# Kernel tuning notes

Measured on AMD Instinct MI355X. Metric: run time of the kernel, lower is better.

## Reference

```python
import jax, jax.numpy as jnp
import numpy as np

HIDDEN = 2048
NUM_HEADS = 16
NUM_KV_HEADS = 4
HEAD_DIM = HIDDEN // NUM_HEADS  # 128
WINDOW = 512
THETA = 10000.0
BATCH = 4
SEQ = 2048
NEG = -1e30


def _apply_rope(x, pos, theta):
    # x: [T, H, D] with interleaved even/odd rotation, matching the torch strided slicing
    half = x.shape[-1] // 2
    inv_freq = 1.0 / (theta ** (jnp.arange(half, dtype=jnp.float32) / half))
    ang = pos.astype(jnp.float32)[:, None] * inv_freq[None, :]          # [T, half]
    cos = jnp.cos(ang)[:, None, :]                                       # [T, 1, half]
    sin = jnp.sin(ang)[:, None, :]
    xe = x[..., 0::2].astype(jnp.float32)
    xo = x[..., 1::2].astype(jnp.float32)
    re = xe * cos - xo * sin
    ro = xe * sin + xo * cos
    out = jnp.stack([re, ro], axis=-1).reshape(x.shape)                  # re-interleave
    return out.astype(x.dtype)


def setup_inputs() -> dict:
    key = jax.random.key(0)
    ks = jax.random.split(key, 5)
    sc = 1.0 / np.sqrt(HIDDEN)
    hidden_states = jax.random.normal(ks[0], (BATCH * SEQ, HIDDEN), dtype=jnp.float32)
    q_w = jax.random.normal(ks[1], (HIDDEN, NUM_HEADS * HEAD_DIM), dtype=jnp.float32) * sc
    k_w = jax.random.normal(ks[2], (HIDDEN, NUM_KV_HEADS * HEAD_DIM), dtype=jnp.float32) * sc
    v_w = jax.random.normal(ks[3], (HIDDEN, NUM_KV_HEADS * HEAD_DIM), dtype=jnp.float32) * sc
    o_w = jax.random.normal(ks[4], (HIDDEN, HIDDEN), dtype=jnp.float32) * sc
    position_ids = jnp.tile(jnp.arange(SEQ, dtype=jnp.int32), BATCH)     # restart per sequence
    cu_seqlens = jnp.arange(BATCH + 1, dtype=jnp.int32) * SEQ
    return {
        "hidden_states": hidden_states, "q_w": q_w, "k_w": k_w, "v_w": v_w, "o_w": o_w,
        "position_ids": position_ids, "cu_seqlens": cu_seqlens, "max_seq_len": SEQ,
    }


def reference(hidden_states, q_w, k_w, v_w, o_w, position_ids, cu_seqlens, max_seq_len):
    T = hidden_states.shape[0]
    B = cu_seqlens.shape[0] - 1
    S = T // B  # equal-length packing
    groups = NUM_HEADS // NUM_KV_HEADS

    q = (hidden_states @ q_w).reshape(T, NUM_HEADS, HEAD_DIM)
    k = (hidden_states @ k_w).reshape(T, NUM_KV_HEADS, HEAD_DIM)
    v = (hidden_states @ v_w).reshape(T, NUM_KV_HEADS, HEAD_DIM)

    q = _apply_rope(q, position_ids, THETA)
    k = _apply_rope(k, position_ids, THETA)

    q = q.reshape(B, S, NUM_HEADS, HEAD_DIM)
    k = k.reshape(B, S, NUM_KV_HEADS, HEAD_DIM)
    v = v.reshape(B, S, NUM_KV_HEADS, HEAD_DIM)
    # GQA: expand kv heads to query heads
    k = jnp.repeat(k, groups, axis=2)   # [B, S, H, D]
    v = jnp.repeat(v, groups, axis=2)

    scale = 1.0 / np.sqrt(HEAD_DIM)
    scores = jnp.einsum('bqhd,bkhd->bhqk', q, k) * scale  # [B, H, S, S]

    pos = position_ids.reshape(B, S)
    pq = pos[:, None, :, None]
    pk = pos[:, None, None, :]
    # causal + sliding window (flash window_size=(WINDOW, 0) semantics): q-k in [0, WINDOW]
    allowed = (pk <= pq) & ((pq - pk) <= WINDOW)
    scores = jnp.where(allowed, scores, NEG)

    probs = jax.nn.softmax(scores, axis=-1)
    attn = jnp.einsum('bhqk,bkhd->bqhd', probs, v)        # [B, S, H, D]
    attn = attn.reshape(T, HIDDEN)
    return attn @ o_w
```

## Files before the change

### kernel.cpp

```cpp
#include <hip/hip_runtime.h>
#include <hip/hip_bf16.h>
#include <cstdint>
#include <cstddef>

typedef __bf16 bf16;
typedef __bf16 bf16x2 __attribute__((ext_vector_type(2)));
typedef __bf16 bf16x8 __attribute__((ext_vector_type(8)));
typedef float  f32x4  __attribute__((ext_vector_type(4)));

#define HIDDEN 2048
#define NHEADS 16
#define NKV    4
#define HD     128
#define WINDOW 512
#define NLT    -0.14390747054172642f

__device__ __forceinline__ void gld16(const void* g, void* s) {
  __builtin_amdgcn_global_load_lds((const __attribute__((address_space(1))) void*)g,
                                   (__attribute__((address_space(3))) void*)s, 16, 0, 0);
}

__device__ __forceinline__ f32x4 mfma16(bf16x8 a, bf16x8 b, f32x4 c) {
  return __builtin_amdgcn_mfma_f32_16x16x32_bf16(a, b, c, 0, 0, 0);
}

__device__ __forceinline__ void barrier_raw() {
  asm volatile("" ::: "memory");
  __builtin_amdgcn_s_barrier();
  asm volatile("" ::: "memory");
}

__global__ __launch_bounds__(256) void cast_f32_bf16(const float* __restrict__ in,
                                                     bf16* __restrict__ out, int n4) {
  int i = blockIdx.x * 256 + threadIdx.x;
  if (i >= n4) return;
  f32x4 v = *(const f32x4*)(in + (size_t)i * 4);
  bf16x2 a, b;
  a[0] = (bf16)v[0]; a[1] = (bf16)v[1];
  b[0] = (bf16)v[2]; b[1] = (bf16)v[3];
  *(bf16x2*)(out + (size_t)i * 4)     = a;
  *(bf16x2*)(out + (size_t)i * 4 + 2) = b;
}

__global__ __launch_bounds__(256) void transpose_cast2(const float* __restrict__ in0,
                                                       bf16* __restrict__ out0,
                                                       const float* __restrict__ in1,
                                                       bf16* __restrict__ out1,
                                                       int R, int C) {
  const float* in = blockIdx.z ? in1 : in0;
  bf16* out       = blockIdx.z ? out1 : out0;
  __shared__ float tile[32][33];
  int c0 = blockIdx.x * 32, r0 = blockIdx.y * 32;
  int tx = threadIdx.x, ty = threadIdx.y;
  #pragma unroll
  for (int i = 0; i < 4; ++i)
    tile[ty + i * 8][tx] = in[(size_t)(r0 + ty + i * 8) * C + c0 + tx];
  __syncthreads();
  #pragma unroll
  for (int i = 0; i < 4; ++i)
    out[(size_t)(c0 + ty + i * 8) * R + r0 + tx] = (bf16)tile[tx][ty + i * 8];
}

__device__ __forceinline__ void stage128x64(const bf16* __restrict__ A,
                                            const bf16* __restrict__ Bt,
                                            bf16* sA, bf16* sB,
                                            int m0, int n0, int K, int kt, int tid) {
  int wb = (tid & ~63) * 8;
  #pragma unroll
  for (int r = 0; r < 4; ++r) {
    int n = r * 256 + tid;
    int row = n >> 3;
    int c = (n & 7) ^ (row & 7);
    gld16(A  + (size_t)(m0 + row) * K + (size_t)kt * 64 + c * 8,
          sA + (size_t)(r * 256 * 8) + wb);
    gld16(Bt + (size_t)(n0 + row) * K + (size_t)kt * 64 + c * 8,
          sB + (size_t)(r * 256 * 8) + wb);
  }
}

__global__ __launch_bounds__(256) void gemm_bt(const bf16* __restrict__ A,
                                               const bf16* __restrict__ Bt,
                                               void* __restrict__ Cv,
                                               bf16* __restrict__ Vtout,
                                               const int* __restrict__ pos,
                                               int M, int N, int K, int outMode) {
  __shared__ bf16 sA[2][128 * 64];
  __shared__ bf16 sB[2][128 * 64];
  int nb = N >> 7;
  int perx = (int)gridDim.x >> 3;
  int bid0 = (int)blockIdx.x;
  int swzb = (bid0 & 7) * perx + (bid0 >> 3);
  int bm = swzb / nb, bn = swzb % nb;
  int m0 = bm << 7, n0 = bn << 7;
  int tid = threadIdx.x;
  int lane = tid & 63, w = tid >> 6;
  int li = lane & 15, g = lane >> 4;
  int wm = w >> 1, wn = w & 1;
  int swz = li & 7;
  f32x4 acc[4][4] = {};
  int NT = K >> 6;

  stage128x64(A, Bt, sA[0], sB[0], m0, n0, K, 0, tid);
  for (int kt = 0; kt < NT; ++kt) {
    int cur = kt & 1;
    asm volatile("s_waitcnt vmcnt(0)" ::: "memory");
    barrier_raw();
    if (kt + 1 < NT)
      stage128x64(A, Bt, sA[cur ^ 1], sB[cur ^ 1], m0, n0, K, kt + 1, tid);
    bf16x8 af[4][2], bv[4][2];
    #pragma unroll
    for (int mt = 0; mt < 4; ++mt)
      #pragma unroll
      for (int ks = 0; ks < 2; ++ks)
        af[mt][ks] = *(const bf16x8*)&sA[cur][(wm * 64 + mt * 16 + li) * 64
                                              + ((ks * 4 + g) ^ swz) * 8];
    #pragma unroll
    for (int nt = 0; nt < 4; ++nt)
      #pragma unroll
      for (int ks = 0; ks < 2; ++ks)
        bv[nt][ks] = *(const bf16x8*)&sB[cur][(wn * 64 + nt * 16 + li) * 64
                                              + ((ks * 4 + g) ^ swz) * 8];
    #pragma unroll
    for (int mt = 0; mt < 4; ++mt)
      #pragma unroll
      for (int nt = 0; nt < 4; ++nt)
        #pragma unroll
        for (int ks = 0; ks < 2; ++ks)
          acc[mt][nt] = mfma16(af[mt][ks], bv[nt][ks], acc[mt][nt]);
  }
  #pragma unroll
  for (int mt = 0; mt < 4; ++mt)
    #pragma unroll
    for (int nt = 0; nt < 4; ++nt)
      #pragma unroll
      for (int j = 0; j < 4; ++j) {
        int row = m0 + wm * 64 + mt * 16 + g * 4 + j;
        int col = n0 + wn * 64 + nt * 16 + li;
        float v = acc[mt][nt][j];
        if (outMode == 0)      ((bf16*)Cv)[(size_t)row * N + col] = (bf16)v;
        else if (outMode == 1) ((bf16*)Cv)[(size_t)col * M + row] = (bf16)v;
        else if (outMode == 2) ((float*)Cv)[(size_t)row * N + col] = v;
        else {
          if (col < 512) {
            float inv = __expf((float)((col & 127) >> 1) * NLT);
            float ang = (float)pos[row] * inv;
            float s = __sinf(ang), c = __cosf(ang);
            float pv = __shfl_xor(v, 1);
            float outv = (li & 1) ? (pv * s + v * c) : (v * c - pv * s);
            ((bf16*)Cv)[(size_t)row * 512 + col] = (bf16)outv;
          } else {
            Vtout[(size_t)(col - 512) * M + row] = (bf16)v;
          }
        }
      }
}

template<int RSP>
__device__ __forceinline__ void stage_quad(const bf16* __restrict__ G,
                                           bf16* __restrict__ sbuf,
                                           int grow0, int K, int k0, int half, int tid) {
  int w = tid >> 6, lane = tid & 63;
  int rl = lane >> 3;
  int col = ((lane & 7) ^ rl) * 8;
  #pragma unroll
  for (int r = 0; r < 2; ++r) {
    int lr0 = r * 64 + w * 8;
    int row0 = (lr0 & (RSP - 1)) + half * RSP + (lr0 / RSP) * 2 * RSP;
    gld16(G + (size_t)(grow0 + row0 + rl) * K + k0 + col,
          sbuf + row0 * 64);
  }
}

__global__ __launch_bounds__(512, 2) void gemm256(const bf16* __restrict__ A,
                                                  const bf16* __restrict__ Bt,
                                                  void* __restrict__ Cv,
                                                  const int* __restrict__ pos,
                                                  int M, int N, int K, int outMode) {
  __shared__ bf16 sA[2][256 * 64];
  __shared__ bf16 sB[2][256 * 64];
  int nb = N >> 8;
  int cpx = (int)gridDim.x >> 3;
  int bid = (int)blockIdx.x;
  int swzb = (bid & 7) * cpx + (bid >> 3);
  int bm = swzb / nb, bn = swzb % nb;
  int m0 = bm << 8, n0 = bn << 8;
  int tid = threadIdx.x, lane = tid & 63, w = tid >> 6;
  int li = lane & 15, g = lane >> 4;
  int wm = w >> 2, wn = w & 3;
  int swz = (li & 7);

  f32x4 acc[8][4] = {};
  bf16x8 af[4][2];
  bf16x8 bv[2][2][2];

  int NT = K >> 6;

  stage_quad<64>(A,  sA[0], m0, K, 0, 0, tid);
  stage_quad<32>(Bt, sB[0], n0, K, 0, 0, tid);
  stage_quad<32>(Bt, sB[0], n0, K, 0, 1, tid);
  stage_quad<64>(A,  sA[0], m0, K, 0, 1, tid);

#define VMW(n) asm volatile("s_waitcnt vmcnt(" #n ")" ::: "memory")
#define SBAR() __builtin_amdgcn_sched_barrier(0)
#define LGKM(n) { asm volatile("s_waitcnt lgkmcnt(" #n ")" ::: "memory"); \
  __builtin_amdgcn_sched_barrier(0); }
#define LOAD_A256(mh) { _Pragma("unroll") for (int mf = 0; mf < 4; ++mf) \
  _Pragma("unroll") for (int ks = 0; ks < 2; ++ks) { \
    int row = wm * 128 + (mh) * 64 + mf * 16 + li; \
    af[mf][ks] = *(const bf16x8*)&sA[cur][row * 64 + ((ks * 4 + g) ^ swz) * 8]; } }
#define LOAD_B256(nh) { _Pragma("unroll") for (int nf = 0; nf < 2; ++nf) \
  _Pragma("unroll") for (int ks = 0; ks < 2; ++ks) { \
    int row = wn * 64 + (nh) * 32 + nf * 16 + li; \
    bv[nh][nf][ks] = *(const bf16x8*)&sB[cur][row * 64 + ((ks * 4 + g) ^ swz) * 8]; } }
#define MFMA_PH(mh, nh) { \
  __builtin_amdgcn_s_setprio(1); \
  _Pragma("unroll") for (int mf = 0; mf < 4; ++mf) \
  _Pragma("unroll") for (int nf = 0; nf < 2; ++nf) \
  _Pragma("unroll") for (int ks = 0; ks < 2; ++ks) \
    acc[(mh) * 4 + mf][(nh) * 2 + nf] = \
      mfma16(af[mf][ks], bv[nh][nf][ks], acc[(mh) * 4 + mf][(nh) * 2 + nf]); \
  __builtin_amdgcn_s_setprio(0); }

  int cur = 0;
  for (int t = 0; t < NT; ++t) {
    int nxt = cur ^ 1;
    bool pre = (t + 1 < NT);
    int k1 = (t + 1) << 6;
    VMW(0);
    barrier_raw();
    if (pre) stage_quad<64>(A, sA[nxt], m0, K, k1, 0, tid);
    LOAD_A256(0); LOAD_B256(0);
    SBAR();
    LOAD_B256(1);
    if (pre) stage_quad<32>(Bt, sB[nxt], n0, K, k1, 0, tid);
    LGKM(4);
    MFMA_PH(0, 0);
    if (pre) stage_quad<32>(Bt, sB[nxt], n0, K, k1, 1, tid);
    LGKM(0);
    MFMA_PH(0, 1);
    LOAD_A256(1);
    if (pre) stage_quad<64>(A, sA[nxt], m0, K, k1, 1, tid);
    LGKM(0);
    MFMA_PH(1, 1);
    MFMA_PH(1, 0);
    cur = nxt;
  }
#undef VMW
#undef SBAR
#undef LGKM
#undef LOAD_A256
#undef LOAD_B256
#undef MFMA_PH

  if (outMode == 3) {
    float inv4[4];
    #pragma unroll
    for (int ni = 0; ni < 4; ++ni) {
      int col = n0 + wn * 64 + ni * 16 + li;
      inv4[ni] = __expf((float)((col & 127) >> 1) * NLT);
    }
    #pragma unroll
    for (int mi = 0; mi < 8; ++mi)
      #pragma unroll
      for (int j = 0; j < 4; ++j) {
        int row = m0 + wm * 128 + mi * 16 + g * 4 + j;
        float pr = (float)pos[row];
        #pragma unroll
        for (int ni = 0; ni < 4; ++ni) {
          int col = n0 + wn * 64 + ni * 16 + li;
          float ang = pr * inv4[ni];
          float s = __sinf(ang), c = __cosf(ang);
          float v = acc[mi][ni][j];
          float pv = __shfl_xor(v, 1);
          float outv = (li & 1) ? (pv * s + v * c) : (v * c - pv * s);
          ((bf16*)Cv)[(size_t)row * N + col] = (bf16)outv;
        }
      }
  } else {
    #pragma unroll
    for (int mi = 0; mi < 8; ++mi)
      #pragma unroll
      for (int ni = 0; ni < 4; ++ni)
        #pragma unroll
        for (int j = 0; j < 4; ++j) {
          int row = m0 + wm * 128 + mi * 16 + g * 4 + j;
          int col = n0 + wn * 64 + ni * 16 + li;
          float v = acc[mi][ni][j];
          if (outMode == 2) ((float*)Cv)[(size_t)row * N + col] = v;
          else              ((bf16*)Cv)[(size_t)row * N + col] = (bf16)v;
        }
  }
}

__global__ __launch_bounds__(512) void attn_kernel(const bf16* __restrict__ Q,
                                                   const bf16* __restrict__ Kb,
                                                   const bf16* __restrict__ Vt,
                                                   const int* __restrict__ pos,
                                                   const int* __restrict__ cu,
                                                   bf16* __restrict__ O, int T, int B) {
  __shared__ bf16 sK[2][64 * 128];
  __shared__ bf16 sV[2][128 * 64];
  __shared__ bf16 sP[8][16 * 40];
  int bid = blockIdx.x;
  int nqb = T >> 6;
  int kvh = bid / nqb;
  int u   = bid % nqb;
  int qb  = (u & 7) * (nqb >> 3) + (u >> 3);
  int q0 = qb * 64;
  int tid = threadIdx.x, lane = tid & 63, w = tid >> 6;
  int hh = w & 3, rh = w >> 2;
  int h = kvh * 4 + hh;
  int li = lane & 15, g = lane >> 4, g8 = g * 8;
  int rb0 = q0 + rh * 32;

  int seq_start = 0, seq_end = T;
  for (int b = 0; b < B; ++b) {
    int a = cu[b], e = cu[b + 1];
    if (q0 >= a && q0 < e) { seq_start = a; seq_end = e; }
  }

  bf16x8 qf[2][4];
  #pragma unroll
  for (int grp = 0; grp < 2; ++grp)
    #pragma unroll
    for (int kd = 0; kd < 4; ++kd)
      qf[grp][kd] = *(const bf16x8*)(Q + (size_t)(rb0 + grp * 16 + li) * HIDDEN
                                     + h * HD + kd * 32 + g8);

  int pq[2][4], pmin[2], pmax[2];
  #pragma unroll
  for (int grp = 0; grp < 2; ++grp) {
    #pragma unroll
    for (int j = 0; j < 4; ++j) pq[grp][j] = pos[rb0 + grp * 16 + g * 4 + j];
    pmin[grp] = pos[rb0 + grp * 16];
    pmax[grp] = pos[rb0 + grp * 16 + 15];
  }

  float lsum[2][4] = {};
  f32x4 acc[2][8] = {};
  int kstart = q0 - WINDOW;
  if (kstart < seq_start) kstart = seq_start;
  int kend = q0 + 64;
  if (kend > seq_end) kend = seq_end;
  const float scale = 0.08838834764831845f;
  int nt = (kend - kstart) >> 6;

#define STAGE(kb_, buf_) { \
  _Pragma("unroll") for (int r = 0; r < 2; ++r) { \
    int n = r * 512 + tid; \
    int krow = n >> 4, kc = (n & 15) ^ (krow & 7); \
    gld16(Kb + (size_t)((kb_) + krow) * (NKV * HD) + kvh * HD + kc * 8, \
          &sK[buf_][(size_t)(r * 512 + (tid & ~63)) * 8]); \
    int vd = n >> 3, vc = (n & 7) ^ (vd & 7); \
    gld16(Vt + (size_t)(kvh * HD + vd) * T + (kb_) + vc * 8, \
          &sV[buf_][(size_t)(r * 512 + (tid & ~63)) * 8]); } }
#define VMW(n) asm volatile("s_waitcnt vmcnt(" #n ")" ::: "memory")

  STAGE(kstart, 0);
  for (int t = 0; t < nt; ++t) {
    int kb0 = kstart + t * 64;
    int cur = t & 1;
    VMW(0);
    barrier_raw();
    if (t + 1 < nt) STAGE(kb0 + 64, cur ^ 1);

    #pragma unroll
    for (int hhalf = 0; hhalf < 2; ++hhalf) {
      int kb = kb0 + hhalf * 32;
      int pkf = pos[kb], pkl = pos[kb + 31];
      int pk0 = pos[kb + li], pk1 = pos[kb + 16 + li];
      #pragma unroll
      for (int grp = 0; grp < 2; ++grp) {
        if (pkf > pmax[grp] || pkl < pmin[grp] - WINDOW) continue;
        f32x4 s0v = {0.f, 0.f, 0.f, 0.f}, s1v = {0.f, 0.f, 0.f, 0.f};
        #pragma unroll
        for (int kd = 0; kd < 4; ++kd) {
          int c0 = (kd * 4 + g) ^ (li & 7);
          bf16x8 b0 = *(const bf16x8*)&sK[cur][(hhalf * 32 + li) * 128 + c0 * 8];
          bf16x8 b1 = *(const bf16x8*)&sK[cur][(hhalf * 32 + 16 + li) * 128 + c0 * 8];
          s0v = mfma16(qf[grp][kd], b0, s0v);
          s1v = mfma16(qf[grp][kd], b1, s1v);
        }
        bool interior = (pkl <= pmin[grp]) && (pmax[grp] - pkf <= WINDOW);
        if (interior) {
          #pragma unroll
          for (int j = 0; j < 4; ++j) {
            float p0 = __expf(s0v[j] * scale);
            float p1 = __expf(s1v[j] * scale);
            lsum[grp][j] += p0 + p1;
            sP[w][(g * 4 + j) * 40 + li]      = (bf16)p0;
            sP[w][(g * 4 + j) * 40 + 16 + li] = (bf16)p1;
          }
        } else {
          #pragma unroll
          for (int j = 0; j < 4; ++j) {
            int d0 = pq[grp][j] - pk0, d1 = pq[grp][j] - pk1;
            float p0 = (d0 >= 0 && d0 <= WINDOW) ? __expf(s0v[j] * scale) : 0.f;
            float p1 = (d1 >= 0 && d1 <= WINDOW) ? __expf(s1v[j] * scale) : 0.f;
            lsum[grp][j] += p0 + p1;
            sP[w][(g * 4 + j) * 40 + li]      = (bf16)p0;
            sP[w][(g * 4 + j) * 40 + 16 + li] = (bf16)p1;
          }
        }
        bf16x8 pa = *(const bf16x8*)&sP[w][li * 40 + g8];
        #pragma unroll
        for (int dt = 0; dt < 8; ++dt) {
          int d = dt * 16 + li;
          int vc2 = (hhalf * 4 + g) ^ (d & 7);
          bf16x8 vf = *(const bf16x8*)&sV[cur][d * 64 + vc2 * 8];
          acc[grp][dt] = mfma16(pa, vf, acc[grp][dt]);
        }
      }
    }
  }
#undef STAGE
#undef VMW

  #pragma unroll
  for (int grp = 0; grp < 2; ++grp)
    #pragma unroll
    for (int j = 0; j < 4; ++j) {
      float rs = lsum[grp][j];
      rs += __shfl_xor(rs, 1);
      rs += __shfl_xor(rs, 2);
      rs += __shfl_xor(rs, 4);
      rs += __shfl_xor(rs, 8);
      float invl = 1.0f / rs;
      size_t base = (size_t)(rb0 + grp * 16 + g * 4 + j) * HIDDEN + h * HD;
      #pragma unroll
      for (int dt = 0; dt < 8; ++dt)
        O[base + dt * 16 + li] = (bf16)(acc[grp][dt][j] * invl);
    }
}

extern "C" void kernel_launch(void* const* d_in, const int* in_sizes, int n_in,
                              void* d_out, int out_size, void* d_ws, size_t ws_size,
                              hipStream_t stream) {
  const float* X  = (const float*)d_in[0];
  const float* qw = (const float*)d_in[1];
  const float* kw = (const float*)d_in[2];
  const float* vw = (const float*)d_in[3];
  const float* ow = (const float*)d_in[4];
  const int* pos = (const int*)d_in[5];
  const int* cu  = (const int*)d_in[6];
  int T = in_sizes[0] / HIDDEN;
  int B = in_sizes[6] - 1;
  float* out = (float*)d_out;

  bf16* ws = (bf16*)d_ws;
  size_t off = 0;
  bf16* Xb    = ws + off; off += (size_t)T * HIDDEN;
  bf16* Qb    = ws + off; off += (size_t)T * HIDDEN;
  bf16* Kb    = ws + off; off += (size_t)T * (NKV * HD);
  bf16* Vt    = ws + off; off += (size_t)T * (NKV * HD);
  bf16* qwT   = ws + off; off += (size_t)HIDDEN * HIDDEN;
  bf16* kvwT  = ws + off; off += (size_t)1024 * HIDDEN;
  bf16* owT   = ws + off; off += (size_t)HIDDEN * HIDDEN;

  cast_f32_bf16<<<(T * HIDDEN / 4 + 255) / 256, 256, 0, stream>>>(X, Xb, T * HIDDEN / 4);

  dim3 tb(32, 8);
  transpose_cast2<<<dim3(HIDDEN / 32, HIDDEN / 32, 2), tb, 0, stream>>>(
      qw, qwT, ow, owT, HIDDEN, HIDDEN);
  transpose_cast2<<<dim3(512 / 32, HIDDEN / 32, 2), tb, 0, stream>>>(
      kw, kvwT, vw, kvwT + (size_t)512 * HIDDEN, HIDDEN, 512);

  gemm256<<<(T / 256) * (HIDDEN / 256), 512, 0, stream>>>(Xb, qwT, Qb, pos,
                                                          T, HIDDEN, HIDDEN, 3);
  gemm_bt<<<(T / 128) * (1024 / 128), 256, 0, stream>>>(Xb, kvwT, Kb, Vt, pos,
                                                        T, 1024, HIDDEN, 3);

  attn_kernel<<<(T / 64) * NKV, 512, 0, stream>>>(Qb, Kb, Vt, pos, cu, Qb, T, B);

  gemm256<<<(T / 256) * (HIDDEN / 256), 512, 0, stream>>>(Qb, owT, out, nullptr,
                                                          T, HIDDEN, HIDDEN, 2);
}
```

Measured before the change: 282.6 us.

## Vectorize cast and epilogue stores, issue all gemm256 prefetches up front

Several changes land together. The f32-to-bf16 cast now handles 8 elements per thread with one 16-byte store, and the gemm_bt epilogue splits by column range. The V part writes 4 contiguous bf16 with one vector store, and the RoPE parts pair neighbouring lanes into bf16x2 stores. The gemm256 main loop now issues all four next-tile global-to-LDS stage loads at the start of each iteration, instead of interleaving them between MFMA phases. This aims to cut the number of narrow stores and to start prefetching earlier, at the risk of bunching memory traffic ahead of the MFMA work.

After: 292.3 us. 3.4% more time.

```diff
diff --git a/kernel.cpp b/kernel.cpp
--- a/kernel.cpp
+++ b/kernel.cpp
@@ -5,6 +5,7 @@
 
 typedef __bf16 bf16;
 typedef __bf16 bf16x2 __attribute__((ext_vector_type(2)));
+typedef __bf16 bf16x4 __attribute__((ext_vector_type(4)));
 typedef __bf16 bf16x8 __attribute__((ext_vector_type(8)));
 typedef float  f32x4  __attribute__((ext_vector_type(4)));
 
@@ -31,15 +32,15 @@
 }
 
 __global__ __launch_bounds__(256) void cast_f32_bf16(const float* __restrict__ in,
-                                                     bf16* __restrict__ out, int n4) {
+                                                     bf16* __restrict__ out, int n8) {
   int i = blockIdx.x * 256 + threadIdx.x;
-  if (i >= n4) return;
-  f32x4 v = *(const f32x4*)(in + (size_t)i * 4);
-  bf16x2 a, b;
-  a[0] = (bf16)v[0]; a[1] = (bf16)v[1];
-  b[0] = (bf16)v[2]; b[1] = (bf16)v[3];
-  *(bf16x2*)(out + (size_t)i * 4)     = a;
-  *(bf16x2*)(out + (size_t)i * 4 + 2) = b;
+  if (i >= n8) return;
+  f32x4 a = *(const f32x4*)(in + (size_t)i * 8);
+  f32x4 b = *(const f32x4*)(in + (size_t)i * 8 + 4);
+  bf16x8 o;
+  #pragma unroll
+  for (int k = 0; k < 4; ++k) { o[k] = (bf16)a[k]; o[k + 4] = (bf16)b[k]; }
+  *(bf16x8*)(out + (size_t)i * 8) = o;
 }
 
 __global__ __launch_bounds__(256) void transpose_cast2(const float* __restrict__ in0,
@@ -128,31 +129,54 @@
         for (int ks = 0; ks < 2; ++ks)
           acc[mt][nt] = mfma16(af[mt][ks], bv[nt][ks], acc[mt][nt]);
   }
-  #pragma unroll
-  for (int mt = 0; mt < 4; ++mt)
-    #pragma unroll
-    for (int nt = 0; nt < 4; ++nt)
-      #pragma unroll
-      for (int j = 0; j < 4; ++j) {
-        int row = m0 + wm * 64 + mt * 16 + g * 4 + j;
+  if (outMode == 3 && n0 >= 512) {
+    #pragma unroll
+    for (int mt = 0; mt < 4; ++mt)
+      #pragma unroll
+      for (int nt = 0; nt < 4; ++nt) {
+        int row0 = m0 + wm * 64 + mt * 16 + g * 4;
         int col = n0 + wn * 64 + nt * 16 + li;
-        float v = acc[mt][nt][j];
-        if (outMode == 0)      ((bf16*)Cv)[(size_t)row * N + col] = (bf16)v;
-        else if (outMode == 1) ((bf16*)Cv)[(size_t)col * M + row] = (bf16)v;
-        else if (outMode == 2) ((float*)Cv)[(size_t)row * N + col] = v;
-        else {
-          if (col < 512) {
-            float inv = __expf((float)((col & 127) >> 1) * NLT);
-            float ang = (float)pos[row] * inv;
-            float s = __sinf(ang), c = __cosf(ang);
-            float pv = __shfl_xor(v, 1);
-            float outv = (li & 1) ? (pv * s + v * c) : (v * c - pv * s);
-            ((bf16*)Cv)[(size_t)row * 512 + col] = (bf16)outv;
-          } else {
-            Vtout[(size_t)(col - 512) * M + row] = (bf16)v;
+        bf16x4 vv;
+        #pragma unroll
+        for (int j = 0; j < 4; ++j) vv[j] = (bf16)acc[mt][nt][j];
+        *(bf16x4*)&Vtout[(size_t)(col - 512) * M + row0] = vv;
+      }
+  } else if (outMode == 3) {
+    #pragma unroll
+    for (int mt = 0; mt < 4; ++mt)
+      #pragma unroll
+      for (int nt = 0; nt < 4; ++nt)
+        #pragma unroll
+        for (int j = 0; j < 4; ++j) {
+          int row = m0 + wm * 64 + mt * 16 + g * 4 + j;
+          int col = n0 + wn * 64 + nt * 16 + li;
+          float v = acc[mt][nt][j];
+          float inv = __expf((float)((col & 127) >> 1) * NLT);
+          float ang = (float)pos[row] * inv;
+          float s = __sinf(ang), c = __cosf(ang);
+          float pv = __shfl_xor(v, 1);
+          float outv = (li & 1) ? (pv * s + v * c) : (v * c - pv * s);
+          float po = __shfl_xor(outv, 1);
+          if (!(lane & 1)) {
+            bf16x2 t2; t2[0] = (bf16)outv; t2[1] = (bf16)po;
+            *(bf16x2*)&((bf16*)Cv)[(size_t)row * 512 + col] = t2;
           }
         }
-      }
+  } else {
+    #pragma unroll
+    for (int mt = 0; mt < 4; ++mt)
+      #pragma unroll
+      for (int nt = 0; nt < 4; ++nt)
+        #pragma unroll
+        for (int j = 0; j < 4; ++j) {
+          int row = m0 + wm * 64 + mt * 16 + g * 4 + j;
+          int col = n0 + wn * 64 + nt * 16 + li;
+          float v = acc[mt][nt][j];
+          if (outMode == 0)      ((bf16*)Cv)[(size_t)row * N + col] = (bf16)v;
+          else if (outMode == 1) ((bf16*)Cv)[(size_t)col * M + row] = (bf16)v;
+          else                   ((float*)Cv)[(size_t)row * N + col] = v;
+        }
+  }
 }
 
 template<int RSP>
@@ -228,18 +252,20 @@
     int k1 = (t + 1) << 6;
     VMW(0);
     barrier_raw();
-    if (pre) stage_quad<64>(A, sA[nxt], m0, K, k1, 0, tid);
+    if (pre) {
+      stage_quad<64>(A,  sA[nxt], m0, K, k1, 0, tid);
+      stage_quad<32>(Bt, sB[nxt], n0, K, k1, 0, tid);
+      stage_quad<32>(Bt, sB[nxt], n0, K, k1, 1, tid);
+      stage_quad<64>(A,  sA[nxt], m0, K, k1, 1, tid);
+    }
     LOAD_A256(0); LOAD_B256(0);
     SBAR();
     LOAD_B256(1);
-    if (pre) stage_quad<32>(Bt, sB[nxt], n0, K, k1, 0, tid);
     LGKM(4);
     MFMA_PH(0, 0);
-    if (pre) stage_quad<32>(Bt, sB[nxt], n0, K, k1, 1, tid);
     LGKM(0);
     MFMA_PH(0, 1);
     LOAD_A256(1);
-    if (pre) stage_quad<64>(A, sA[nxt], m0, K, k1, 1, tid);
     LGKM(0);
     MFMA_PH(1, 1);
     MFMA_PH(1, 0);
@@ -273,7 +299,11 @@
           float v = acc[mi][ni][j];
           float pv = __shfl_xor(v, 1);
           float outv = (li & 1) ? (pv * s + v * c) : (v * c - pv * s);
-          ((bf16*)Cv)[(size_t)row * N + col] = (bf16)outv;
+          float po = __shfl_xor(outv, 1);
+          if (!(lane & 1)) {
+            bf16x2 t2; t2[0] = (bf16)outv; t2[1] = (bf16)po;
+            *(bf16x2*)&((bf16*)Cv)[(size_t)row * N + col] = t2;
+          }
         }
       }
   } else {
@@ -457,7 +487,7 @@
   bf16* kvwT  = ws + off; off += (size_t)1024 * HIDDEN;
   bf16* owT   = ws + off; off += (size_t)HIDDEN * HIDDEN;
 
-  cast_f32_bf16<<<(T * HIDDEN / 4 + 255) / 256, 256, 0, stream>>>(X, Xb, T * HIDDEN / 4);
+  cast_f32_bf16<<<(T * HIDDEN / 8 + 255) / 256, 256, 0, stream>>>(X, Xb, T * HIDDEN / 8);
 
   dim3 tb(32, 8);
   transpose_cast2<<<dim3(HIDDEN / 32, HIDDEN / 32, 2), tb, 0, stream>>>(
```
